# Optimization experiments

Measured on AMD Instinct MI355X. Metric: run time of the kernel, lower is better.

The kernel has to match this reference:

```python
import jax, jax.numpy as jnp
import numpy as np

R = 8      # num_dilation_rates
B = 32
C_IN = 21
C = 128    # C_out
L = 4096
K = 2      # kernel_size


def _causal_conv(x, w, dilation, pad, length):
    # x: [B, C, L], w: [Co, Ci, K]. Left-pad by `pad`, dilated valid conv, keep first L.
    # Matches Causal_conv1d: type 'A' -> pad=K(=2); type 'B' -> pad=dilation*(K-1)+1.
    y = jax.lax.conv_general_dilated(
        x, w, window_strides=(1,), padding=[(pad, 0)],
        rhs_dilation=(dilation,), dimension_numbers=('NCH', 'OIH', 'NCH'))
    return y[:, :, :length]


def setup_inputs() -> dict:
    key = jax.random.key(0)
    ks = jax.random.split(key, 10)
    s = 0.1  # small init scale (stands in for xavier)
    return {
        'x': jax.random.normal(ks[0], (B, C_IN, L), jnp.float32),
        'z': jax.random.normal(ks[1], (B, 1, L), jnp.float32),
        'w0': jax.random.normal(ks[2], (C, C_IN), jnp.float32) * s,          # causal_blocks[0] 1x1 conv
        'b0': jnp.zeros((C,), jnp.float32),
        'signal_w': jax.random.normal(ks[3], (R, C, C, K), jnp.float32) * s,  # dilated kernel-2 convs
        'gate_w': jax.random.normal(ks[4], (R, C, C, K), jnp.float32) * s,
        'cond_signal_w': jax.random.normal(ks[5], (R, C), jnp.float32) * s,   # Conv1d(1, C, 1) weights
        'cond_gate_w': jax.random.normal(ks[6], (R, C), jnp.float32) * s,
        'res_w': jax.random.normal(ks[7], (R, C, C), jnp.float32) * s,        # 1x1 residual convs
        'skip_w': jax.random.normal(ks[8], (R, C, C), jnp.float32) * s,       # 1x1 skip convs
    }


def reference(x, z, w0, b0, signal_w, gate_w, cond_signal_w, cond_gate_w, res_w, skip_w):
    length = x.shape[2]
    # initial 1x1 conv with bias
    h = jnp.einsum('oi,bil->bol', w0, x) + b0[None, :, None]
    orig = h
    cum_skip = jnp.zeros_like(h)
    zf = z[:, 0, :]  # [B, L]
    n_rates = signal_w.shape[0]
    for ii in range(n_rates):
        d = 2 ** ii
        pad = K if ii == 0 else d * (K - 1) + 1  # mask 'A' for layer 0, 'B' otherwise
        signal = _causal_conv(h, signal_w[ii], d, pad, length) \
            + jnp.einsum('o,bl->bol', cond_signal_w[ii], zf)
        gate = _causal_conv(h, gate_w[ii], d, pad, length) \
            + jnp.einsum('o,bl->bol', cond_gate_w[ii], zf)
        g = signal * jax.nn.sigmoid(gate)                      # gated activation
        skip = jnp.einsum('oi,bil->bol', skip_w[ii], g)
        res = jnp.einsum('oi,bil->bol', res_w[ii], g)
        h = (orig + res) if ii == 0 else (res + g)             # matches torch control flow
        cum_skip = cum_skip + skip
    return h, cum_skip
```

## Files before the change

### kernel.cpp

```cpp
#include <hip/hip_runtime.h>
#include <hip/hip_bf16.h>

#define RR 8
#define BB 32
#define CIN 21
#define CC 128
#define LL 4096
#define TT 64
#define GP 136
#define PADT 132
#define LP (LL + PADT)

typedef short s16x8 __attribute__((ext_vector_type(8)));
typedef float f32x4 __attribute__((ext_vector_type(4)));
typedef unsigned int __attribute__((address_space(1))) gu32;
typedef unsigned int __attribute__((address_space(3))) lu32;

__device__ __forceinline__ unsigned short f2b(float f) {
    __hip_bfloat16 h = __float2bfloat16(f);
    return *reinterpret_cast<unsigned short*>(&h);
}
__device__ __forceinline__ float b2f(unsigned short u) {
    __hip_bfloat16 h;
    *reinterpret_cast<unsigned short*>(&h) = u;
    return __bfloat162float(h);
}
__device__ __forceinline__ unsigned int packsplit(float v) {
    unsigned short hi = f2b(v);
    unsigned short lo = f2b(v - b2f(hi));
    return ((unsigned int)hi << 16) | (unsigned int)lo;
}
__device__ __forceinline__ float unpacksum(unsigned int u) {
    return b2f((unsigned short)(u >> 16)) + b2f((unsigned short)(u & 0xffffu));
}

__device__ __forceinline__ void unpack2(uint4 u0, uint4 u1, s16x8& hi, s16x8& lo) {
    union { int i[4]; s16x8 v; } H, L;
    H.i[0] = __builtin_amdgcn_perm(u0.y, u0.x, 0x07060302u);
    L.i[0] = __builtin_amdgcn_perm(u0.y, u0.x, 0x05040100u);
    H.i[1] = __builtin_amdgcn_perm(u0.w, u0.z, 0x07060302u);
    L.i[1] = __builtin_amdgcn_perm(u0.w, u0.z, 0x05040100u);
    H.i[2] = __builtin_amdgcn_perm(u1.y, u1.x, 0x07060302u);
    L.i[2] = __builtin_amdgcn_perm(u1.y, u1.x, 0x05040100u);
    H.i[3] = __builtin_amdgcn_perm(u1.w, u1.z, 0x07060302u);
    L.i[3] = __builtin_amdgcn_perm(u1.w, u1.z, 0x05040100u);
    hi = H.v; lo = L.v;
}

__global__ void prep_kernel(const float* __restrict__ sw, const float* __restrict__ gw,
                            const float* __restrict__ skw, const float* __restrict__ rew,
                            unsigned short* __restrict__ WsgH, unsigned short* __restrict__ WsgL,
                            unsigned short* __restrict__ WkrH, unsigned short* __restrict__ WkrL) {
    int idx = blockIdx.x * 256 + threadIdx.x;
    int r = idx >> 16;
    int rem = idx & 65535;
    int o = rem >> 8;
    int k = rem & 255;
    int c = k & 127;
    int tap = k >> 7;
    float v = (o < 128) ? sw[(((r * 128 + o) * 128 + c) << 1) + tap]
                        : gw[(((r * 128 + (o - 128)) * 128 + c) << 1) + tap];
    unsigned short hi = f2b(v);
    WsgH[idx] = hi;
    WsgL[idx] = f2b(v - b2f(hi));
    if (idx < RR * 256 * 128) {
        int r2 = idx >> 15;
        int rem2 = idx & 32767;
        int o2 = rem2 >> 7;
        int c2 = rem2 & 127;
        float v2 = (o2 < 128) ? skw[(r2 * 128 + o2) * 128 + c2]
                              : rew[(r2 * 128 + (o2 - 128)) * 128 + c2];
        unsigned short hi2 = f2b(v2);
        WkrH[idx] = hi2;
        WkrL[idx] = f2b(v2 - b2f(hi2));
    }
}

__global__ void zero_pad_kernel(unsigned int* __restrict__ hA, unsigned int* __restrict__ hB) {
    int idx = blockIdx.x * 256 + threadIdx.x;
    int c = idx & 127;
    int r = (idx >> 7) % PADT;
    int b = idx / (PADT * 128);
    size_t off = ((size_t)b * LP + r) * CC + c;
    hA[off] = 0u;
    hB[off] = 0u;
}

__global__ void proj_kernel(const float* __restrict__ x, const float* __restrict__ w0,
                            const float* __restrict__ b0, unsigned int* __restrict__ h0) {
    int idx = blockIdx.x * 256 + threadIdx.x;
    int c = idx & 127;
    int t = (idx >> 7) & (LL - 1);
    int b = idx >> 19;
    const float* xb = x + (size_t)b * CIN * LL + t;
    const float* w = w0 + c * CIN;
    float acc = b0[c];
#pragma unroll
    for (int i = 0; i < CIN; i++) acc = fmaf(w[i], xb[i * LL], acc);
    h0[((size_t)b * LP + PADT + t) * CC + c] = packsplit(acc);
}

__global__ void __launch_bounds__(512, 4) layer_kernel(
    const unsigned int* __restrict__ hcur,
    unsigned int* __restrict__ hnext,
    float* __restrict__ skipbuf,
    const unsigned short* __restrict__ WsgH, const unsigned short* __restrict__ WsgL,
    const unsigned short* __restrict__ WkrH, const unsigned short* __restrict__ WkrL,
    const float* __restrict__ csw, const float* __restrict__ cgw,
    const float* __restrict__ z,
    float* __restrict__ out,
    int off0, int first, int last) {
    __shared__ unsigned int sBuf[16384];
    unsigned short* sGhi = (unsigned short*)sBuf;
    unsigned short* sGlo = sGhi + TT * GP;

    int tid = threadIdx.x;
    int b = blockIdx.x >> 6;
    int t0 = (blockIdx.x & 63) * TT;

    int wave = tid >> 6;
    int lane = tid & 63;
    int l15 = lane & 15;
    int quad = lane >> 4;

    const unsigned int* hb = hcur + (size_t)b * LP * CC;
    const int cch = wave * 16 + l15;

    {
        const unsigned int* src0 = hb + (size_t)(PADT + t0 - off0) * CC;
        const unsigned int* src1 = hb + (size_t)(PADT + t0 - 1) * CC;
#pragma unroll
        for (int jj = 0; jj < 8; jj++) {
            int flat = tid + 512 * jj;
            int row = (flat >> 5) & 63;
            int ud = flat & 31;
            const unsigned int* srcw = (jj < 4) ? src0 : src1;
            const unsigned int* gp = srcw + (size_t)row * CC + ((ud ^ (row & 7)) << 2);
            __builtin_amdgcn_global_load_lds((const gu32*)gp, (lu32*)(sBuf + flat * 4), 16, 0, 0);
        }
    }
    __syncthreads();

    f32x4 acc1[4][2];
#pragma unroll
    for (int m = 0; m < 4; m++)
#pragma unroll
        for (int n = 0; n < 2; n++) acc1[m][n] = (f32x4){0.f, 0.f, 0.f, 0.f};

    {
        const int o0 = (wave + 0) * 16 + l15;
        const int o1 = (wave + 8) * 16 + l15;
        s16x8 Bh[2][2], Bl[2][2];
#pragma unroll
        for (int n = 0; n < 2; n++) {
            int o = n ? o1 : o0;
            Bh[0][n] = *(const s16x8*)(WsgH + o * 256 + quad * 8);
            Bl[0][n] = *(const s16x8*)(WsgL + o * 256 + quad * 8);
        }
#pragma unroll
        for (int kk = 0; kk < 8; kk++) {
            const int cur = kk & 1, nxt = cur ^ 1;
            if (kk < 7) {
#pragma unroll
                for (int n = 0; n < 2; n++) {
                    int o = n ? o1 : o0;
                    Bh[nxt][n] = *(const s16x8*)(WsgH + o * 256 + (kk + 1) * 32 + quad * 8);
                    Bl[nxt][n] = *(const s16x8*)(WsgL + o * 256 + (kk + 1) * 32 + quad * 8);
                }
            }
            const int win = kk >> 2;
            const int U = (kk & 3) * 8 + quad * 2;
            s16x8 Ah[4], Al[4];
#pragma unroll
            for (int m = 0; m < 4; m++) {
                int r = m * 16 + l15;
                const unsigned int* base = sBuf + win * 8192 + r * 128;
                int s = r & 7;
                uint4 x0 = *(const uint4*)(base + ((U ^ s) << 2));
                uint4 x1 = *(const uint4*)(base + (((U + 1) ^ s) << 2));
                unpack2(x0, x1, Ah[m], Al[m]);
            }
            __builtin_amdgcn_s_setprio(1);
#pragma unroll
            for (int n = 0; n < 2; n++)
#pragma unroll
                for (int m = 0; m < 4; m++) {
                    acc1[m][n] = __builtin_amdgcn_mfma_f32_16x16x32_bf16(Ah[m], Bh[cur][n], acc1[m][n], 0, 0, 0);
                    acc1[m][n] = __builtin_amdgcn_mfma_f32_16x16x32_bf16(Al[m], Bh[cur][n], acc1[m][n], 0, 0, 0);
                    acc1[m][n] = __builtin_amdgcn_mfma_f32_16x16x32_bf16(Ah[m], Bl[cur][n], acc1[m][n], 0, 0, 0);
                }
            __builtin_amdgcn_s_setprio(0);
        }
    }

    __syncthreads();
    {
        const float* zb = z + (size_t)b * LL + t0;
        float cs = csw[cch];
        float cg = cgw[cch];
#pragma unroll
        for (int m = 0; m < 4; m++)
#pragma unroll
            for (int reg = 0; reg < 4; reg++) {
                float zv = zb[m * 16 + quad * 4 + reg];
                float s = fmaf(cs, zv, acc1[m][0][reg]);
                float t = fmaf(cg, zv, acc1[m][1][reg]);
                float gv = s / (1.f + __expf(-t));
                int tl = m * 16 + quad * 4 + reg;
                unsigned short hi = f2b(gv);
                sGhi[tl * GP + cch] = hi;
                sGlo[tl * GP + cch] = f2b(gv - b2f(hi));
            }
    }
    __syncthreads();

    f32x4 acc2[4][2];
#pragma unroll
    for (int m = 0; m < 4; m++)
#pragma unroll
        for (int n = 0; n < 2; n++) acc2[m][n] = (f32x4){0.f, 0.f, 0.f, 0.f};

    {
        const int o0 = (wave + 0) * 16 + l15;
        const int o1 = (wave + 8) * 16 + l15;
        s16x8 Bh[2][2], Bl[2][2];
#pragma unroll
        for (int n = 0; n < 2; n++) {
            int o = n ? o1 : o0;
            Bh[0][n] = *(const s16x8*)(WkrH + o * 128 + quad * 8);
            Bl[0][n] = *(const s16x8*)(WkrL + o * 128 + quad * 8);
        }
#pragma unroll
        for (int kk = 0; kk < 4; kk++) {
            const int cur = kk & 1, nxt = cur ^ 1;
            if (kk < 3) {
#pragma unroll
                for (int n = 0; n < 2; n++) {
                    int o = n ? o1 : o0;
                    Bh[nxt][n] = *(const s16x8*)(WkrH + o * 128 + (kk + 1) * 32 + quad * 8);
                    Bl[nxt][n] = *(const s16x8*)(WkrL + o * 128 + (kk + 1) * 32 + quad * 8);
                }
            }
            s16x8 Ah[4], Al[4];
#pragma unroll
            for (int m = 0; m < 4; m++) {
                int off = (m * 16 + l15) * GP + kk * 32 + quad * 8;
                Ah[m] = *(const s16x8*)(sGhi + off);
                Al[m] = *(const s16x8*)(sGlo + off);
            }
            __builtin_amdgcn_s_setprio(1);
#pragma unroll
            for (int n = 0; n < 2; n++)
#pragma unroll
                for (int m = 0; m < 4; m++) {
                    acc2[m][n] = __builtin_amdgcn_mfma_f32_16x16x32_bf16(Ah[m], Bh[cur][n], acc2[m][n], 0, 0, 0);
                    acc2[m][n] = __builtin_amdgcn_mfma_f32_16x16x32_bf16(Al[m], Bh[cur][n], acc2[m][n], 0, 0, 0);
                    acc2[m][n] = __builtin_amdgcn_mfma_f32_16x16x32_bf16(Ah[m], Bl[cur][n], acc2[m][n], 0, 0, 0);
                }
            __builtin_amdgcn_s_setprio(0);
        }
    }

#pragma unroll
    for (int m = 0; m < 4; m++) {
#pragma unroll
        for (int reg = 0; reg < 4; reg++) {
            int tl = m * 16 + quad * 4 + reg;
            int t = t0 + tl;
            size_t hidx = ((size_t)b * LP + PADT + t) * CC + cch;
            size_t sidx = ((size_t)b * LL + t) * CC + cch;
            float skp = acc2[m][0][reg];
            float res = acc2[m][1][reg];
            float hv, sv;
            if (first) {
                hv = res + unpacksum(hcur[hidx]);
                sv = skp;
            } else {
                hv = res + b2f(sGhi[tl * GP + cch]) + b2f(sGlo[tl * GP + cch]);
                sv = skp + skipbuf[sidx];
            }
            if (last) {
                size_t oidx = ((size_t)b * CC + cch) * LL + t;
                out[oidx] = hv;
                out[(size_t)BB * CC * LL + oidx] = sv;
            } else {
                hnext[hidx] = packsplit(hv);
                skipbuf[sidx] = sv;
            }
        }
    }
}

extern "C" void kernel_launch(void* const* d_in, const int* in_sizes, int n_in,
                              void* d_out, int out_size, void* d_ws, size_t ws_size,
                              hipStream_t stream) {
    const float* x = (const float*)d_in[0];
    const float* z = (const float*)d_in[1];
    const float* w0 = (const float*)d_in[2];
    const float* b0 = (const float*)d_in[3];
    const float* sw = (const float*)d_in[4];
    const float* gw = (const float*)d_in[5];
    const float* csw = (const float*)d_in[6];
    const float* cgw = (const float*)d_in[7];
    const float* rew = (const float*)d_in[8];
    const float* skw = (const float*)d_in[9];

    const size_t HSZ = (size_t)BB * LP * CC;
    const size_t NCL = (size_t)BB * CC * LL;
    unsigned int* hA = (unsigned int*)d_ws;
    unsigned int* hB = hA + HSZ;
    float* skipb = (float*)(hB + HSZ);
    unsigned short* WsgH = (unsigned short*)(skipb + NCL);
    unsigned short* WsgL = WsgH + (size_t)RR * 256 * 256;
    unsigned short* WkrH = WsgL + (size_t)RR * 256 * 256;
    unsigned short* WkrL = WkrH + (size_t)RR * 256 * 128;

    prep_kernel<<<RR * 256 * 256 / 256, 256, 0, stream>>>(sw, gw, skw, rew, WsgH, WsgL, WkrH, WkrL);
    zero_pad_kernel<<<BB * PADT * 128 / 256, 256, 0, stream>>>(hA, hB);
    proj_kernel<<<NCL / 256, 256, 0, stream>>>(x, w0, b0, hA);

    unsigned int* hc = hA;
    unsigned int* hn = hB;
    for (int ii = 0; ii < RR; ii++) {
        int d = 1 << ii;
        int off0 = d + 1;
        layer_kernel<<<BB * (LL / TT), 512, 0, stream>>>(
            hc, hn, skipb,
            WsgH + (size_t)ii * 256 * 256, WsgL + (size_t)ii * 256 * 256,
            WkrH + (size_t)ii * 256 * 128, WkrL + (size_t)ii * 256 * 128,
            csw + ii * CC, cgw + ii * CC, z,
            (float*)d_out, off0, ii == 0 ? 1 : 0, ii == RR - 1 ? 1 : 0);
        unsigned int* tmp = hc; hc = hn; hn = tmp;
    }
}
```

Measured before the change: 1.343 ms.

## Load a single overlapping input window for small dilations to shrink LDS

For layers whose dilation offset is at most 33, the layer kernel now stages one contiguous window of 64+off0 rows instead of two separate 64-row windows. The two conv taps then read shifted rows of that shared buffer. This cuts global-to-LDS traffic and shrinks shared memory to 97 rows, which allows a higher occupancy hint (6 blocks per CU). Larger dilations keep the original two-window kernel as layerB. The cost is a duplicated kernel and conditional loads, and the 97-row LDS buffer must still hold the later gated-activation staging.

```diff
diff --git a/kernel.cpp b/kernel.cpp
--- a/kernel.cpp
+++ b/kernel.cpp
@@ -10,6 +10,7 @@
 #define GP 136
 #define PADT 132
 #define LP (LL + PADT)
+#define URMAX 97
 
 typedef short s16x8 __attribute__((ext_vector_type(8)));
 typedef float f32x4 __attribute__((ext_vector_type(4)));
@@ -100,7 +101,8 @@
     h0[((size_t)b * LP + PADT + t) * CC + c] = packsplit(acc);
 }
 
-__global__ void __launch_bounds__(512, 4) layer_kernel(
+
+__global__ void __launch_bounds__(512, 6) layerA_kernel(
     const unsigned int* __restrict__ hcur,
     unsigned int* __restrict__ hnext,
     float* __restrict__ skipbuf,
@@ -110,7 +112,7 @@
     const float* __restrict__ z,
     float* __restrict__ out,
     int off0, int first, int last) {
-    __shared__ unsigned int sBuf[16384];
+    __shared__ unsigned int sBuf[URMAX * 128];
     unsigned short* sGhi = (unsigned short*)sBuf;
     unsigned short* sGlo = sGhi + TT * GP;
 
@@ -127,16 +129,17 @@
     const int cch = wave * 16 + l15;
 
     {
-        const unsigned int* src0 = hb + (size_t)(PADT + t0 - off0) * CC;
-        const unsigned int* src1 = hb + (size_t)(PADT + t0 - 1) * CC;
-#pragma unroll
-        for (int jj = 0; jj < 8; jj++) {
+        const unsigned int* srcU = hb + (size_t)(PADT + t0 - off0) * CC;
+        int nunits = (64 + off0) * 32;
+#pragma unroll
+        for (int jj = 0; jj < 7; jj++) {
             int flat = tid + 512 * jj;
-            int row = (flat >> 5) & 63;
-            int ud = flat & 31;
-            const unsigned int* srcw = (jj < 4) ? src0 : src1;
-            const unsigned int* gp = srcw + (size_t)row * CC + ((ud ^ (row & 7)) << 2);
-            __builtin_amdgcn_global_load_lds((const gu32*)gp, (lu32*)(sBuf + flat * 4), 16, 0, 0);
+            if (flat < nunits) {
+                int row = flat >> 5;
+                int ud = flat & 31;
+                const unsigned int* gp = srcU + (size_t)row * CC + ((ud ^ (row & 7)) << 2);
+                __builtin_amdgcn_global_load_lds((const gu32*)gp, (lu32*)(sBuf + flat * 4), 16, 0, 0);
+            }
         }
     }
     __syncthreads();
@@ -168,14 +171,14 @@
                     Bl[nxt][n] = *(const s16x8*)(WsgL + o * 256 + (kk + 1) * 32 + quad * 8);
                 }
             }
-            const int win = kk >> 2;
+            const int rbase = (kk >> 2) ? (off0 - 1) : 0;
             const int U = (kk & 3) * 8 + quad * 2;
             s16x8 Ah[4], Al[4];
 #pragma unroll
             for (int m = 0; m < 4; m++) {
-                int r = m * 16 + l15;
-                const unsigned int* base = sBuf + win * 8192 + r * 128;
-                int s = r & 7;
+                int srow = m * 16 + l15 + rbase;
+                const unsigned int* base = sBuf + srow * 128;
+                int s = srow & 7;
                 uint4 x0 = *(const uint4*)(base + ((U ^ s) << 2));
                 uint4 x1 = *(const uint4*)(base + (((U + 1) ^ s) << 2));
                 unpack2(x0, x1, Ah[m], Al[m]);
@@ -291,6 +294,197 @@
     }
 }
 
+__global__ void __launch_bounds__(512, 4) layerB_kernel(
+    const unsigned int* __restrict__ hcur,
+    unsigned int* __restrict__ hnext,
+    float* __restrict__ skipbuf,
+    const unsigned short* __restrict__ WsgH, const unsigned short* __restrict__ WsgL,
+    const unsigned short* __restrict__ WkrH, const unsigned short* __restrict__ WkrL,
+    const float* __restrict__ csw, const float* __restrict__ cgw,
+    const float* __restrict__ z,
+    float* __restrict__ out,
+    int off0, int first, int last) {
+    __shared__ unsigned int sBuf[16384];
+    unsigned short* sGhi = (unsigned short*)sBuf;
+    unsigned short* sGlo = sGhi + TT * GP;
+
+    int tid = threadIdx.x;
+    int b = blockIdx.x >> 6;
+    int t0 = (blockIdx.x & 63) * TT;
+
+    int wave = tid >> 6;
+    int lane = tid & 63;
+    int l15 = lane & 15;
+    int quad = lane >> 4;
+
+    const unsigned int* hb = hcur + (size_t)b * LP * CC;
+    const int cch = wave * 16 + l15;
+
+    {
+        const unsigned int* src0 = hb + (size_t)(PADT + t0 - off0) * CC;
+        const unsigned int* src1 = hb + (size_t)(PADT + t0 - 1) * CC;
+#pragma unroll
+        for (int jj = 0; jj < 8; jj++) {
+            int flat = tid + 512 * jj;
+            int row = (flat >> 5) & 63;
+            int ud = flat & 31;
+            const unsigned int* srcw = (jj < 4) ? src0 : src1;
+            const unsigned int* gp = srcw + (size_t)row * CC + ((ud ^ (row & 7)) << 2);
+            __builtin_amdgcn_global_load_lds((const gu32*)gp, (lu32*)(sBuf + flat * 4), 16, 0, 0);
+        }
+    }
+    __syncthreads();
+
+    f32x4 acc1[4][2];
+#pragma unroll
+    for (int m = 0; m < 4; m++)
+#pragma unroll
+        for (int n = 0; n < 2; n++) acc1[m][n] = (f32x4){0.f, 0.f, 0.f, 0.f};
+
+    {
+        const int o0 = (wave + 0) * 16 + l15;
+        const int o1 = (wave + 8) * 16 + l15;
+        s16x8 Bh[2][2], Bl[2][2];
+#pragma unroll
+        for (int n = 0; n < 2; n++) {
+            int o = n ? o1 : o0;
+            Bh[0][n] = *(const s16x8*)(WsgH + o * 256 + quad * 8);
+            Bl[0][n] = *(const s16x8*)(WsgL + o * 256 + quad * 8);
+        }
+#pragma unroll
+        for (int kk = 0; kk < 8; kk++) {
+            const int cur = kk & 1, nxt = cur ^ 1;
+            if (kk < 7) {
+#pragma unroll
+                for (int n = 0; n < 2; n++) {
+                    int o = n ? o1 : o0;
+                    Bh[nxt][n] = *(const s16x8*)(WsgH + o * 256 + (kk + 1) * 32 + quad * 8);
+                    Bl[nxt][n] = *(const s16x8*)(WsgL + o * 256 + (kk + 1) * 32 + quad * 8);
+                }
+            }
+            const int win = kk >> 2;
+            const int U = (kk & 3) * 8 + quad * 2;
+            s16x8 Ah[4], Al[4];
+#pragma unroll
+            for (int m = 0; m < 4; m++) {
+                int r = m * 16 + l15;
+                const unsigned int* base = sBuf + win * 8192 + r * 128;
+                int s = r & 7;
+                uint4 x0 = *(const uint4*)(base + ((U ^ s) << 2));
+                uint4 x1 = *(const uint4*)(base + (((U + 1) ^ s) << 2));
+                unpack2(x0, x1, Ah[m], Al[m]);
+            }
+            __builtin_amdgcn_s_setprio(1);
+#pragma unroll
+            for (int n = 0; n < 2; n++)
+#pragma unroll
+                for (int m = 0; m < 4; m++) {
+                    acc1[m][n] = __builtin_amdgcn_mfma_f32_16x16x32_bf16(Ah[m], Bh[cur][n], acc1[m][n], 0, 0, 0);
+                    acc1[m][n] = __builtin_amdgcn_mfma_f32_16x16x32_bf16(Al[m], Bh[cur][n], acc1[m][n], 0, 0, 0);
+                    acc1[m][n] = __builtin_amdgcn_mfma_f32_16x16x32_bf16(Ah[m], Bl[cur][n], acc1[m][n], 0, 0, 0);
+                }
+            __builtin_amdgcn_s_setprio(0);
+        }
+    }
+
+    __syncthreads();
+    {
+        const float* zb = z + (size_t)b * LL + t0;
+        float cs = csw[cch];
+        float cg = cgw[cch];
+#pragma unroll
+        for (int m = 0; m < 4; m++)
+#pragma unroll
+            for (int reg = 0; reg < 4; reg++) {
+                float zv = zb[m * 16 + quad * 4 + reg];
+                float s = fmaf(cs, zv, acc1[m][0][reg]);
+                float t = fmaf(cg, zv, acc1[m][1][reg]);
+                float gv = s / (1.f + __expf(-t));
+                int tl = m * 16 + quad * 4 + reg;
+                unsigned short hi = f2b(gv);
+                sGhi[tl * GP + cch] = hi;
+                sGlo[tl * GP + cch] = f2b(gv - b2f(hi));
+            }
+    }
+    __syncthreads();
+
+    f32x4 acc2[4][2];
+#pragma unroll
+    for (int m = 0; m < 4; m++)
+#pragma unroll
+        for (int n = 0; n < 2; n++) acc2[m][n] = (f32x4){0.f, 0.f, 0.f, 0.f};
+
+    {
+        const int o0 = (wave + 0) * 16 + l15;
+        const int o1 = (wave + 8) * 16 + l15;
+        s16x8 Bh[2][2], Bl[2][2];
+#pragma unroll
+        for (int n = 0; n < 2; n++) {
+            int o = n ? o1 : o0;
+            Bh[0][n] = *(const s16x8*)(WkrH + o * 128 + quad * 8);
+            Bl[0][n] = *(const s16x8*)(WkrL + o * 128 + quad * 8);
+        }
+#pragma unroll
+        for (int kk = 0; kk < 4; kk++) {
+            const int cur = kk & 1, nxt = cur ^ 1;
+            if (kk < 3) {
+#pragma unroll
+                for (int n = 0; n < 2; n++) {
+                    int o = n ? o1 : o0;
+                    Bh[nxt][n] = *(const s16x8*)(WkrH + o * 128 + (kk + 1) * 32 + quad * 8);
+                    Bl[nxt][n] = *(const s16x8*)(WkrL + o * 128 + (kk + 1) * 32 + quad * 8);
+                }
+            }
+            s16x8 Ah[4], Al[4];
+#pragma unroll
+            for (int m = 0; m < 4; m++) {
+                int off = (m * 16 + l15) * GP + kk * 32 + quad * 8;
+                Ah[m] = *(const s16x8*)(sGhi + off);
+                Al[m] = *(const s16x8*)(sGlo + off);
+            }
+            __builtin_amdgcn_s_setprio(1);
+#pragma unroll
+            for (int n = 0; n < 2; n++)
+#pragma unroll
+                for (int m = 0; m < 4; m++) {
+                    acc2[m][n] = __builtin_amdgcn_mfma_f32_16x16x32_bf16(Ah[m], Bh[cur][n], acc2[m][n], 0, 0, 0);
+                    acc2[m][n] = __builtin_amdgcn_mfma_f32_16x16x32_bf16(Al[m], Bh[cur][n], acc2[m][n], 0, 0, 0);
+                    acc2[m][n] = __builtin_amdgcn_mfma_f32_16x16x32_bf16(Ah[m], Bl[cur][n], acc2[m][n], 0, 0, 0);
+                }
+            __builtin_amdgcn_s_setprio(0);
+        }
+    }
+
+#pragma unroll
+    for (int m = 0; m < 4; m++) {
+#pragma unroll
+        for (int reg = 0; reg < 4; reg++) {
+            int tl = m * 16 + quad * 4 + reg;
+            int t = t0 + tl;
+            size_t hidx = ((size_t)b * LP + PADT + t) * CC + cch;
+            size_t sidx = ((size_t)b * LL + t) * CC + cch;
+            float skp = acc2[m][0][reg];
+            float res = acc2[m][1][reg];
+            float hv, sv;
+            if (first) {
+                hv = res + unpacksum(hcur[hidx]);
+                sv = skp;
+            } else {
+                hv = res + b2f(sGhi[tl * GP + cch]) + b2f(sGlo[tl * GP + cch]);
+                sv = skp + skipbuf[sidx];
+            }
+            if (last) {
+                size_t oidx = ((size_t)b * CC + cch) * LL + t;
+                out[oidx] = hv;
+                out[(size_t)BB * CC * LL + oidx] = sv;
+            } else {
+                hnext[hidx] = packsplit(hv);
+                skipbuf[sidx] = sv;
+            }
+        }
+    }
+}
+
 extern "C" void kernel_launch(void* const* d_in, const int* in_sizes, int n_in,
                               void* d_out, int out_size, void* d_ws, size_t ws_size,
                               hipStream_t stream) {
@@ -324,12 +518,21 @@
     for (int ii = 0; ii < RR; ii++) {
         int d = 1 << ii;
         int off0 = d + 1;
-        layer_kernel<<<BB * (LL / TT), 512, 0, stream>>>(
-            hc, hn, skipb,
-            WsgH + (size_t)ii * 256 * 256, WsgL + (size_t)ii * 256 * 256,
-            WkrH + (size_t)ii * 256 * 128, WkrL + (size_t)ii * 256 * 128,
-            csw + ii * CC, cgw + ii * CC, z,
-            (float*)d_out, off0, ii == 0 ? 1 : 0, ii == RR - 1 ? 1 : 0);
+        if (off0 <= 33) {
+            layerA_kernel<<<BB * (LL / TT), 512, 0, stream>>>(
+                hc, hn, skipb,
+                WsgH + (size_t)ii * 256 * 256, WsgL + (size_t)ii * 256 * 256,
+                WkrH + (size_t)ii * 256 * 128, WkrL + (size_t)ii * 256 * 128,
+                csw + ii * CC, cgw + ii * CC, z,
+                (float*)d_out, off0, ii == 0 ? 1 : 0, ii == RR - 1 ? 1 : 0);
+        } else {
+            layerB_kernel<<<BB * (LL / TT), 512, 0, stream>>>(
+                hc, hn, skipb,
+                WsgH + (size_t)ii * 256 * 256, WsgL + (size_t)ii * 256 * 256,
+                WkrH + (size_t)ii * 256 * 128, WkrL + (size_t)ii * 256 * 128,
+                csw + ii * CC, cgw + ii * CC, z,
+                (float*)d_out, off0, ii == 0 ? 1 : 0, ii == RR - 1 ? 1 : 0);
+        }
         unsigned int* tmp = hc; hc = hn; hn = tmp;
     }
 }
```

Result: slower. 3.718 ms (+176.9%).
